# Kernel tuning notes

Hardware: AMD Instinct MI355X
Metric: run time of the kernel (lower is better)

The kernel has to match this reference:

```python
import jax, jax.numpy as jnp
import numpy as np

H = 12
DH = 64
R = 8
LN_EPS = 1e-12


def setup_inputs() -> dict:
    key = jax.random.key(0)
    ks = jax.random.split(key, 6)
    B, T, D = 32, 512, 768
    s = 0.02  # realistic init scale so softmax/LN stay well-conditioned
    return {
        "hidden_states": jax.random.normal(ks[0], (B, T, D), jnp.float32),
        "Wq": jax.random.normal(ks[1], (D, D), jnp.float32) * s,
        "bq": jnp.zeros((D,), jnp.float32),
        "Wk": jax.random.normal(ks[2], (D, D), jnp.float32) * s,
        "bk": jnp.zeros((D,), jnp.float32),
        "Wv": jax.random.normal(ks[3], (D, D), jnp.float32) * s,
        "bv": jnp.zeros((D,), jnp.float32),
        "Wo": jax.random.normal(ks[4], (D, D), jnp.float32) * s,
        "bo": jnp.zeros((D,), jnp.float32),
        "ln_g": jnp.ones((D,), jnp.float32),
        "ln_b": jnp.zeros((D,), jnp.float32),
    }


def _bipartite_indices(metric, r):
    # metric: (B, T, dh); cosine-sim bipartite matching between even (a) and odd (b) tokens
    m = metric / (jnp.linalg.norm(metric, axis=-1, keepdims=True) + 1e-6)
    a, b = m[:, ::2], m[:, 1::2]
    scores = jnp.einsum('bad,bcd->bac', a, b)  # (B, Ta, Tb)
    node_max = scores.max(axis=-1)
    node_idx = scores.argmax(axis=-1)
    node_max = node_max.at[:, 0].set(-jnp.inf)  # protect CLS (a[0])
    r = min(r, a.shape[1] - 1)
    sorted_idx = jnp.argsort(-node_max, axis=-1)  # descending
    src_idx = sorted_idx[:, :r]
    unm_idx = sorted_idx[:, r:]
    dst_idx = jnp.take_along_axis(node_idx, src_idx, axis=-1)
    return src_idx, unm_idx, dst_idx


def _merge(x, src_idx, unm_idx, dst_idx):
    # x: (B, T, C) -> (B, T - r, C); scatter-mean matched even tokens into odd tokens
    src, dst = x[:, ::2], x[:, 1::2]
    matched = jnp.take_along_axis(src, src_idx[:, :, None], axis=1)  # (B, r, C)

    def scat(d, di, mm):
        sums = jnp.zeros_like(d).at[di].add(mm)
        cnt = jnp.zeros((d.shape[0],), d.dtype).at[di].add(jnp.ones(di.shape, d.dtype))
        # torch scatter_reduce 'mean' with include_self=True: (self + sum) / (1 + count)
        return (d + sums) / (1.0 + cnt[:, None])

    dst = jax.vmap(scat)(dst, dst_idx, matched)
    unm = jnp.take_along_axis(src, unm_idx[:, :, None], axis=1)
    return jnp.concatenate([unm, dst], axis=1)


def reference(hidden_states, Wq, bq, Wk, bk, Wv, bv, Wo, bo, ln_g, ln_b):
    B, T, D = hidden_states.shape

    def split_heads(x):
        return x.reshape(B, T, H, DH).transpose(0, 2, 1, 3)  # (B, H, T, dh)

    residual = hidden_states
    q = split_heads(hidden_states @ Wq + bq)
    k = split_heads(hidden_states @ Wk + bk)
    v = split_heads(hidden_states @ Wv + bv)

    # ToMe: match on head-averaged keys (computed under no_grad in torch)
    metric = jax.lax.stop_gradient(k.mean(axis=1))  # (B, T, dh)
    src_idx, unm_idx, dst_idx = _bipartite_indices(metric, R)

    def merge_heads(x):
        Bx, Hx, Tx, dx = x.shape
        y = x.transpose(0, 2, 1, 3).reshape(Bx, Tx, Hx * dx)
        y = _merge(y, src_idx, unm_idx, dst_idx)
        return y.reshape(Bx, y.shape[1], Hx, dx).transpose(0, 2, 1, 3)

    q = merge_heads(q)
    k = merge_heads(k)
    v = merge_heads(v)
    residual = _merge(residual, src_idx, unm_idx, dst_idx)

    scores = jnp.einsum('bhqd,bhkd->bhqk', q, k) / jnp.sqrt(jnp.float32(DH))
    probs = jax.nn.softmax(scores, axis=-1)  # dropout is identity in eval
    ctx = jnp.einsum('bhqk,bhkd->bhqd', probs, v)
    T2 = ctx.shape[2]
    ctx = ctx.transpose(0, 2, 1, 3).reshape(B, T2, D)
    out = ctx @ Wo + bo

    x = out + residual
    mu = x.mean(axis=-1, keepdims=True)
    var = x.var(axis=-1, keepdims=True)
    return (x - mu) / jnp.sqrt(var + LN_EPS) * ln_g + ln_b
```

## Files before the change

kernel.cpp:

```cpp
#include <hip/hip_runtime.h>
#include <math.h>

#define BNUM 32
#define TT   512
#define DD   768
#define HH   12
#define DHH  64
#define RR   8
#define TSRC 256
#define UNM  248
#define TM   504
#define MROW 16128

typedef unsigned short u16;
typedef unsigned int   u32;
typedef __attribute__((ext_vector_type(8))) short bfrag;
typedef __attribute__((ext_vector_type(4))) float ffrag;

__device__ __forceinline__ u16 f2bf(float f) {
  u32 u = __float_as_uint(f);
  u = (u + 0x7fffu + ((u >> 16) & 1u)) >> 16;
  return (u16)u;
}
__device__ __forceinline__ u32 pack2bf(float a, float b) {
  u32 ua = __float_as_uint(a), ub = __float_as_uint(b);
  ua += 0x7fffu + ((ua >> 16) & 1u);
  ub += 0x7fffu + ((ub >> 16) & 1u);
  return (ua >> 16) | (ub & 0xffff0000u);
}
__device__ __forceinline__ float bf2f(u16 v) {
  return __uint_as_float(((u32)v) << 16);
}

__device__ __forceinline__ void gl2lds16(const u16* g, u16* l) {
  __builtin_amdgcn_global_load_lds(
      (const __attribute__((address_space(1))) void*)(g),
      (__attribute__((address_space(3))) void*)(l), 16, 0, 0);
}

__global__ __launch_bounds__(256) void wkr_kernel(
    const float* __restrict__ Wk, const float* __restrict__ bk,
    float* __restrict__ Wkr, float* __restrict__ bkr) {
  int idx = blockIdx.x * 256 + threadIdx.x;
  int d = idx >> 6, j = idx & 63;
  float s = 0.f;
  #pragma unroll
  for (int h = 0; h < HH; ++h) s += Wk[(size_t)d * DD + h * DHH + j];
  Wkr[idx] = s * (1.f / 12.f);
  if (idx < 64) {
    float sb = 0.f;
    #pragma unroll
    for (int h = 0; h < HH; ++h) sb += bk[h * DHH + idx];
    bkr[idx] = sb * (1.f / 12.f);
  }
}

__global__ __launch_bounds__(256) void gemm_f32_kernel(
    const float* __restrict__ A, const float* __restrict__ W,
    const float* __restrict__ bias, float* __restrict__ C,
    int M, int N, int K) {
  __shared__ float As[32][34];
  __shared__ float Ws[32][66];
  const int t  = threadIdx.x;
  const int m0 = blockIdx.x * 32;
  const int tx = t & 15, ty = t >> 4;
  const int a_kk = t & 31;
  const int a_m  = t >> 5;
  const int w_n  = t & 63;
  const int w_k0 = t >> 6;

  float a_pre[4], w_pre[8];
  #pragma unroll
  for (int l = 0; l < 4; ++l)
    a_pre[l] = A[(size_t)(m0 + a_m + 8 * l) * K + a_kk];
  #pragma unroll
  for (int l = 0; l < 8; ++l)
    w_pre[l] = W[(size_t)(w_k0 * 8 + l) * N + w_n];

  float4 acc0 = make_float4(0.f, 0.f, 0.f, 0.f);
  float4 acc1 = make_float4(0.f, 0.f, 0.f, 0.f);

  for (int k0 = 0; k0 < K; k0 += 32) {
    __syncthreads();
    #pragma unroll
    for (int l = 0; l < 4; ++l) As[a_kk][a_m + 8 * l] = a_pre[l];
    #pragma unroll
    for (int l = 0; l < 8; ++l) Ws[w_k0 * 8 + l][w_n] = w_pre[l];
    __syncthreads();
    if (k0 + 32 < K) {
      #pragma unroll
      for (int l = 0; l < 4; ++l)
        a_pre[l] = A[(size_t)(m0 + a_m + 8 * l) * K + k0 + 32 + a_kk];
      #pragma unroll
      for (int l = 0; l < 8; ++l)
        w_pre[l] = W[(size_t)(k0 + 32 + w_k0 * 8 + l) * N + w_n];
    }
    #pragma unroll
    for (int kk = 0; kk < 32; ++kk) {
      float2 a2 = *(const float2*)&As[kk][ty * 2];
      float4 w4 = *(const float4*)&Ws[kk][tx * 4];
      acc0.x += a2.x * w4.x; acc0.y += a2.x * w4.y; acc0.z += a2.x * w4.z; acc0.w += a2.x * w4.w;
      acc1.x += a2.y * w4.x; acc1.y += a2.y * w4.y; acc1.z += a2.y * w4.z; acc1.w += a2.y * w4.w;
    }
  }
  const float4 b4 = *(const float4*)&bias[tx * 4];
  float4 v0 = acc0, v1 = acc1;
  v0.x += b4.x; v0.y += b4.y; v0.z += b4.z; v0.w += b4.w;
  v1.x += b4.x; v1.y += b4.y; v1.z += b4.z; v1.w += b4.w;
  *(float4*)&C[(size_t)(m0 + ty * 2) * N + tx * 4]     = v0;
  *(float4*)&C[(size_t)(m0 + ty * 2 + 1) * N + tx * 4] = v1;
}

__global__ __launch_bounds__(256) void wconv_kernel(
    const float* __restrict__ W0, const float* __restrict__ W1,
    const float* __restrict__ W2, const float* __restrict__ W3,
    u16* __restrict__ T0, u16* __restrict__ T1,
    u16* __restrict__ T2, u16* __restrict__ T3) {
  __shared__ float tile[64][65];
  int wi = blockIdx.z;
  const float* W = (wi == 0) ? W0 : (wi == 1) ? W1 : (wi == 2) ? W2 : W3;
  u16* T = (wi == 0) ? T0 : (wi == 1) ? T1 : (wi == 2) ? T2 : T3;
  int k0 = blockIdx.x * 64, n0 = blockIdx.y * 64;
  int t = threadIdx.x;
  int r = t >> 2, c4 = (t & 3) * 16;
  #pragma unroll
  for (int j = 0; j < 16; j += 4) {
    float4 v = *(const float4*)&W[(size_t)(k0 + r) * DD + n0 + c4 + j];
    tile[r][c4 + j] = v.x; tile[r][c4 + j + 1] = v.y;
    tile[r][c4 + j + 2] = v.z; tile[r][c4 + j + 3] = v.w;
  }
  __syncthreads();
  #pragma unroll
  for (int j = 0; j < 16; j += 2) {
    u32 p = (u32)f2bf(tile[c4 + j][r]) | ((u32)f2bf(tile[c4 + j + 1][r]) << 16);
    *(u32*)&T[(size_t)(n0 + r) * DD + k0 + c4 + j] = p;
  }
}

template <bool OUT_BF16, bool ADD_RES, bool ROW_BIAS>
__global__ __launch_bounds__(256) void mfma_gemm_kernel(
    const u16* __restrict__ A, const u16* __restrict__ BT,
    const float* __restrict__ bias, const float* __restrict__ Res,
    float* __restrict__ Cf, u16* __restrict__ Cb,
    int M, int N, int K) {
  __shared__ u16 Als[128 * 64];
  __shared__ u16 Bls[128 * 64];
  const int t  = threadIdx.x;
  const int m0 = blockIdx.x * 128;
  const int n0 = blockIdx.y * 128;
  const int lane = t & 63;
  const int w  = t >> 6;
  const int wm = w & 1, wn = w >> 1;
  const int q  = lane >> 4;
  const int lr = lane & 15;

  const int srow = lane >> 3;
  const int schk = (lane & 7) ^ srow;
  const u16* gA = A  + (size_t)(m0 + w * 32 + srow) * K + schk * 8;
  const u16* gB = BT + (size_t)(n0 + w * 32 + srow) * K + schk * 8;
  u16* lA = &Als[(w * 32) * 64];
  u16* lB = &Bls[(w * 32) * 64];

  const int rchk0 = (q)     ^ (lr & 7);
  const int rchk1 = (4 + q) ^ (lr & 7);

  ffrag acc[4][4];
  #pragma unroll
  for (int i = 0; i < 4; ++i)
    #pragma unroll
    for (int j = 0; j < 4; ++j) {
      acc[i][j].x = 0.f; acc[i][j].y = 0.f; acc[i][j].z = 0.f; acc[i][j].w = 0.f;
    }

  for (int k0 = 0; k0 < K; k0 += 64) {
    __syncthreads();
    #pragma unroll
    for (int i = 0; i < 4; ++i) {
      gl2lds16(gA + (size_t)(i * 8) * K + k0, lA + i * 8 * 64);
      gl2lds16(gB + (size_t)(i * 8) * K + k0, lB + i * 8 * 64);
    }
    __syncthreads();

    bfrag af[2][4], bfv[2][4];
    #pragma unroll
    for (int mi = 0; mi < 4; ++mi) {
      const u16* ra = &Als[(wm * 64 + mi * 16 + lr) * 64];
      af[0][mi] = *(const bfrag*)(ra + rchk0 * 8);
      af[1][mi] = *(const bfrag*)(ra + rchk1 * 8);
    }
    #pragma unroll
    for (int ni = 0; ni < 4; ++ni) {
      const u16* rb = &Bls[(wn * 64 + ni * 16 + lr) * 64];
      bfv[0][ni] = *(const bfrag*)(rb + rchk0 * 8);
      bfv[1][ni] = *(const bfrag*)(rb + rchk1 * 8);
    }
    #pragma unroll
    for (int s = 0; s < 2; ++s)
      #pragma unroll
      for (int mi = 0; mi < 4; ++mi)
        #pragma unroll
        for (int ni = 0; ni < 4; ++ni)
          acc[mi][ni] = __builtin_amdgcn_mfma_f32_16x16x32_bf16(
              af[s][mi], bfv[s][ni], acc[mi][ni], 0, 0, 0);
  }

  float bcol[4];
  if (!ROW_BIAS) {
    #pragma unroll
    for (int ni = 0; ni < 4; ++ni)
      bcol[ni] = bias[n0 + wn * 64 + ni * 16 + lr];
  }

  #pragma unroll
  for (int mi = 0; mi < 4; ++mi) {
    #pragma unroll
    for (int ni = 0; ni < 4; ++ni) {
      int gcol = n0 + wn * 64 + ni * 16 + lr;
      #pragma unroll
      for (int r = 0; r < 4; ++r) {
        int grow = m0 + wm * 64 + mi * 16 + q * 4 + r;
        size_t off = (size_t)grow * N + gcol;
        float v = acc[mi][ni][r];
        v += ROW_BIAS ? bias[grow] : bcol[ni];
        if (ADD_RES) v += Res[off];
        if (OUT_BF16) Cb[off] = f2bf(v);
        else          Cf[off] = v;
      }
    }
  }
}

__global__ __launch_bounds__(256) void tome_kernel(
    const float* __restrict__ metric, int* __restrict__ order_g,
    int* __restrict__ dst_g) {
  __shared__ float sm[TSRC * 64];
  int b = blockIdx.x, i = threadIdx.x;
  const float* Mb = metric + (size_t)b * TT * 64;

  float areg[64];
  float na = 0.f;
  #pragma unroll
  for (int d = 0; d < 64; ++d) {
    float v = Mb[(size_t)(2 * i) * 64 + d];
    areg[d] = v; na += v * v;
  }
  float ia = 1.f / (sqrtf(na) + 1e-6f);
  #pragma unroll
  for (int d = 0; d < 64; ++d) areg[d] *= ia;

  float nb = 0.f;
  #pragma unroll
  for (int d = 0; d < 64; ++d) {
    float v = Mb[(size_t)(2 * i + 1) * 64 + d];
    sm[i * 64 + d] = v; nb += v * v;
  }
  float ib = 1.f / (sqrtf(nb) + 1e-6f);
  #pragma unroll
  for (int d = 0; d < 64; ++d) sm[i * 64 + d] *= ib;
  __syncthreads();

  float best = -INFINITY; int besti = 0;
  for (int c = 0; c < TSRC; ++c) {
    float s = 0.f;
    #pragma unroll
    for (int d = 0; d < 64; ++d) s += areg[d] * sm[c * 64 + d];
    if (s > best) { best = s; besti = c; }
  }
  if (i == 0) best = -INFINITY;
  __syncthreads();

  sm[i] = best;
  int* smi = (int*)(sm + TSRC);
  smi[i] = besti;
  __syncthreads();

  float ki = sm[i];
  int r = 0;
  for (int j = 0; j < TSRC; ++j) {
    float kj = sm[j];
    if (kj > ki || (kj == ki && j < i)) ++r;
  }
  int* ord = smi + TSRC;
  ord[r] = i;
  __syncthreads();

  order_g[b * TSRC + i] = ord[i];
  if (i < RR) dst_g[b * RR + i] = smi[ord[i]];
}

__global__ __launch_bounds__(256) void merge_kernel(
    const float* __restrict__ X, const int* __restrict__ order,
    const int* __restrict__ dsti, float* __restrict__ Xm,
    u16* __restrict__ Xmb) {
  int row = blockIdx.x;
  int b = row / TM, t2 = row % TM;
  int c = threadIdx.x;
  const float* Xb = X + (size_t)b * TT * DD;
  float out[3];
  if (t2 < UNM) {
    int tok = 2 * order[b * TSRC + RR + t2];
    #pragma unroll
    for (int l = 0; l < 3; ++l) out[l] = Xb[(size_t)tok * DD + c + 256 * l];
  } else {
    int j = t2 - UNM;
    float cnt = 1.f;
    #pragma unroll
    for (int l = 0; l < 3; ++l) out[l] = Xb[(size_t)(2 * j + 1) * DD + c + 256 * l];
    for (int m = 0; m < RR; ++m) {
      if (dsti[b * RR + m] == j) {
        int tok = 2 * order[b * TSRC + m];
        #pragma unroll
        for (int l = 0; l < 3; ++l) out[l] += Xb[(size_t)tok * DD + c + 256 * l];
        cnt += 1.f;
      }
    }
    float inv = 1.f / cnt;
    #pragma unroll
    for (int l = 0; l < 3; ++l) out[l] *= inv;
  }
  #pragma unroll
  for (int l = 0; l < 3; ++l) {
    Xm[(size_t)row * DD + c + 256 * l]  = out[l];
    Xmb[(size_t)row * DD + c + 256 * l] = f2bf(out[l]);
  }
}

#define NQT 8
__global__ __launch_bounds__(256) void attn_kernel(
    const u16* __restrict__ Q, const u16* __restrict__ K,
    const u16* __restrict__ VT, u16* __restrict__ ctx) {
  __shared__ u16 Kls[2][64][64];
  __shared__ u16 Vls[2][64][64];
  __shared__ u16 Pt[64][72];

  int blk = blockIdx.x;
  int bh = blk % (BNUM * HH);
  int qt = blk / (BNUM * HH);
  int h = bh % HH, b = bh / HH;
  const int t = threadIdx.x;
  const int lane = t & 63, w = t >> 6;
  const int lr = lane & 15, quad = lane >> 4;
  const int q0 = qt * 64;
  const size_t base = (size_t)b * TM * DD + (size_t)h * DHH;

  bfrag qf[2];
  {
    const u16* qp = Q + base + (size_t)(q0 + 16 * w + lr) * DD + quad * 8;
    qf[0] = *(const bfrag*)(qp);
    qf[1] = *(const bfrag*)(qp + 32);
  }

  const int srow = lane >> 3;
  const int schk = (lane & 7) ^ srow;
  const u16* Kg = K + base + (size_t)schk * 8;
  const u16* Vg0 = VT + (size_t)(h * DHH + w * 16 + srow) * MROW + (size_t)b * TM;
  const u16* Vg1 = Vg0 + (size_t)8 * MROW;

  const int cA = (quad)     ^ (lr & 7);
  const int cB = (quad + 4) ^ (lr & 7);

  float m_i = -INFINITY, l_i = 0.f;
  ffrag o[4];
  #pragma unroll
  for (int ni = 0; ni < 4; ++ni) {
    o[ni].x = 0.f; o[ni].y = 0.f; o[ni].z = 0.f; o[ni].w = 0.f;
  }

  auto STAGE = [&](int cur, int kt) {
    const int k0s = kt * 64;
    int t0 = k0s + w * 16 + srow;
    int t1 = t0 + 8;
    t0 = (t0 < TM) ? t0 : (TM - 1);
    t1 = (t1 < TM) ? t1 : (TM - 1);
    gl2lds16(Kg + (size_t)t0 * DD, &Kls[cur][w * 16][0]);
    gl2lds16(Kg + (size_t)t1 * DD, &Kls[cur][w * 16 + 8][0]);
    int tb = k0s + schk * 8;
    tb = (tb <= TM - 8) ? tb : (TM - 8);
    gl2lds16(Vg0 + tb, &Vls[cur][w * 16][0]);
    gl2lds16(Vg1 + tb, &Vls[cur][w * 16 + 8][0]);
  };

  STAGE(0, 0);
  __syncthreads();

  const float L2E = 1.4426950408889634f;
  const float C1  = 0.125f * 1.4426950408889634f;

  #pragma unroll
  for (int kt = 0; kt < NQT; ++kt) {
    const int cur = kt & 1;

    if (kt + 1 < NQT) STAGE(cur ^ 1, kt + 1);

    ffrag s4[4];
    __builtin_amdgcn_s_setprio(1);
    #pragma unroll
    for (int mi = 0; mi < 4; ++mi) {
      bfrag ka0 = *(const bfrag*)&Kls[cur][mi * 16 + lr][cA * 8];
      bfrag ka1 = *(const bfrag*)&Kls[cur][mi * 16 + lr][cB * 8];
      ffrag z; z.x = 0.f; z.y = 0.f; z.z = 0.f; z.w = 0.f;
      z = __builtin_amdgcn_mfma_f32_16x16x32_bf16(ka0, qf[0], z, 0, 0, 0);
      s4[mi] = __builtin_amdgcn_mfma_f32_16x16x32_bf16(ka1, qf[1], z, 0, 0, 0);
    }
    __builtin_amdgcn_s_setprio(0);

    if (kt == NQT - 1) {
      #pragma unroll
      for (int mi = 0; mi < 4; ++mi)
        #pragma unroll
        for (int r = 0; r < 4; ++r) {
          int rel = mi * 16 + quad * 4 + r;
          if (mi == 3)
            s4[mi][r] = (448 + rel < TM) ? s4[mi][r] : -INFINITY;
        }
    }

    float mx01 = fmaxf(fmaxf(s4[0][0], s4[0][1]), fmaxf(s4[0][2], s4[0][3]));
    float mx23 = fmaxf(fmaxf(s4[1][0], s4[1][1]), fmaxf(s4[1][2], s4[1][3]));
    float mx45 = fmaxf(fmaxf(s4[2][0], s4[2][1]), fmaxf(s4[2][2], s4[2][3]));
    float mx67 = fmaxf(fmaxf(s4[3][0], s4[3][1]), fmaxf(s4[3][2], s4[3][3]));
    float rmax = fmaxf(fmaxf(mx01, mx23), fmaxf(mx45, mx67));
    rmax = fmaxf(rmax, __shfl_xor(rmax, 16));
    rmax = fmaxf(rmax, __shfl_xor(rmax, 32));
    float nm = fmaxf(m_i, rmax * 0.125f);
    float alpha = __builtin_amdgcn_exp2f((m_i - nm) * L2E);
    float nml2 = nm * L2E;

    float p[16];
    float pa0 = 0.f, pa1 = 0.f, pa2 = 0.f, pa3 = 0.f;
    #pragma unroll
    for (int mi = 0; mi < 4; ++mi)
      #pragma unroll
      for (int r = 0; r < 4; ++r) {
        float e = __builtin_amdgcn_exp2f(__builtin_fmaf(s4[mi][r], C1, -nml2));
        p[mi * 4 + r] = e;
        if (r == 0) pa0 += e; else if (r == 1) pa1 += e;
        else if (r == 2) pa2 += e; else pa3 += e;
      }
    float psum = (pa0 + pa1) + (pa2 + pa3);
    psum += __shfl_xor(psum, 16);
    psum += __shfl_xor(psum, 32);
    l_i = l_i * alpha + psum;
    m_i = nm;

    #pragma unroll
    for (int mi = 0; mi < 4; ++mi) {
      u32 lo = pack2bf(p[mi * 4 + 0], p[mi * 4 + 1]);
      u32 hi = pack2bf(p[mi * 4 + 2], p[mi * 4 + 3]);
      u32* dst = (u32*)&Pt[16 * w + lr][mi * 16 + quad * 4];
      dst[0] = lo; dst[1] = hi;
    }

    float al[4];
    #pragma unroll
    for (int r = 0; r < 4; ++r) al[r] = __shfl(alpha, quad * 4 + r);
    #pragma unroll
    for (int ni = 0; ni < 4; ++ni)
      #pragma unroll
      for (int r = 0; r < 4; ++r) o[ni][r] *= al[r];

    bfrag pfa0 = *(const bfrag*)&Pt[16 * w + lr][quad * 8];
    bfrag pfa1 = *(const bfrag*)&Pt[16 * w + lr][32 + quad * 8];
    __builtin_amdgcn_s_setprio(1);
    #pragma unroll
    for (int ni = 0; ni < 4; ++ni) {
      bfrag vb0 = *(const bfrag*)&Vls[cur][ni * 16 + lr][cA * 8];
      bfrag vb1 = *(const bfrag*)&Vls[cur][ni * 16 + lr][cB * 8];
      o[ni] = __builtin_amdgcn_mfma_f32_16x16x32_bf16(pfa0, vb0, o[ni], 0, 0, 0);
      o[ni] = __builtin_amdgcn_mfma_f32_16x16x32_bf16(pfa1, vb1, o[ni], 0, 0, 0);
    }
    __builtin_amdgcn_s_setprio(0);

    __syncthreads();
  }

  float invl[4];
  #pragma unroll
  for (int r = 0; r < 4; ++r) {
    float lv = __shfl(l_i, quad * 4 + r);
    invl[r] = 1.f / lv;
  }
  #pragma unroll
  for (int r = 0; r < 4; ++r) {
    int row = q0 + 16 * w + quad * 4 + r;
    if (row < TM) {
      size_t g = base + (size_t)row * DD + lr;
      #pragma unroll
      for (int ni = 0; ni < 4; ++ni)
        ctx[g + ni * 16] = f2bf(o[ni][r] * invl[r]);
    }
  }
}

__global__ __launch_bounds__(256) void ln_kernel(
    float* __restrict__ Y, const float* __restrict__ g,
    const float* __restrict__ beta) {
  __shared__ float red[4];
  int row = blockIdx.x, t = threadIdx.x;
  size_t baseo = (size_t)row * DD;
  float x[3];
  #pragma unroll
  for (int l = 0; l < 3; ++l) x[l] = Y[baseo + t + 256 * l];
  float s = x[0] + x[1] + x[2];
  #pragma unroll
  for (int off = 32; off > 0; off >>= 1) s += __shfl_down(s, off, 64);
  if ((t & 63) == 0) red[t >> 6] = s;
  __syncthreads();
  float mu = (red[0] + red[1] + red[2] + red[3]) * (1.f / 768.f);
  __syncthreads();
  float d0 = x[0] - mu, d1 = x[1] - mu, d2 = x[2] - mu;
  float sq = d0 * d0 + d1 * d1 + d2 * d2;
  #pragma unroll
  for (int off = 32; off > 0; off >>= 1) sq += __shfl_down(sq, off, 64);
  if ((t & 63) == 0) red[t >> 6] = sq;
  __syncthreads();
  float var = (red[0] + red[1] + red[2] + red[3]) * (1.f / 768.f);
  float inv = rsqrtf(var + 1e-12f);
  #pragma unroll
  for (int l = 0; l < 3; ++l) {
    int c = t + 256 * l;
    Y[baseo + c] = (x[l] - mu) * inv * g[c] + beta[c];
  }
}

extern "C" void kernel_launch(void* const* d_in, const int* in_sizes, int n_in,
                              void* d_out, int out_size, void* d_ws, size_t ws_size,
                              hipStream_t stream) {
  const float* X    = (const float*)d_in[0];
  const float* Wq   = (const float*)d_in[1];
  const float* bq   = (const float*)d_in[2];
  const float* Wk   = (const float*)d_in[3];
  const float* bk   = (const float*)d_in[4];
  const float* Wv   = (const float*)d_in[5];
  const float* bv   = (const float*)d_in[6];
  const float* Wo   = (const float*)d_in[7];
  const float* bo   = (const float*)d_in[8];
  const float* ln_g = (const float*)d_in[9];
  const float* ln_b = (const float*)d_in[10];
  float* out = (float*)d_out;

  const size_t metric_n = (size_t)16384 * 64;
  const size_t wkr_n    = (size_t)768 * 64 + 64;
  const size_t idx_n    = (size_t)BNUM * TSRC + BNUM * RR;
  const size_t buf_n    = (size_t)MROW * DD;
  const size_t w_n      = (size_t)DD * DD;
  const size_t f32_elems = metric_n + wkr_n + idx_n + buf_n;
  const size_t u16_elems = 4 * buf_n + 4 * w_n;
  const size_t needed = f32_elems * 4 + u16_elems * 2;
  if (ws_size < needed) return;

  float* ws = (float*)d_ws;
  float* metric  = ws;
  float* Wkr     = metric + metric_n;
  float* bkr     = Wkr + (size_t)768 * 64;
  int*   order_g = (int*)(bkr + 64);
  int*   dst_g   = order_g + BNUM * TSRC;
  float* Xm      = (float*)(dst_g + BNUM * RR);
  u16*   Xmb     = (u16*)(Xm + buf_n);
  u16*   Qmb     = Xmb + buf_n;
  u16*   Kmb     = Qmb + buf_n;
  u16*   VTb     = Kmb + buf_n;
  u16*   WqT     = VTb + buf_n;
  u16*   WkT     = WqT + w_n;
  u16*   WvT     = WkT + w_n;
  u16*   WoT     = WvT + w_n;
  u16*   ctxb    = Qmb;

  wkr_kernel<<<(768 * 64) / 256, 256, 0, stream>>>(Wk, bk, Wkr, bkr);
  wconv_kernel<<<dim3(12, 12, 4), 256, 0, stream>>>(
      Wq, Wk, Wv, Wo, WqT, WkT, WvT, WoT);
  gemm_f32_kernel<<<dim3(16384 / 32, 1), 256, 0, stream>>>(
      X, Wkr, bkr, metric, 16384, 64, 768);
  tome_kernel<<<BNUM, 256, 0, stream>>>(metric, order_g, dst_g);
  merge_kernel<<<MROW, 256, 0, stream>>>(X, order_g, dst_g, Xm, Xmb);
  mfma_gemm_kernel<true, false, false><<<dim3(MROW / 128, DD / 128), 256, 0, stream>>>(
      Xmb, WqT, bq, nullptr, nullptr, Qmb, MROW, DD, DD);
  mfma_gemm_kernel<true, false, false><<<dim3(MROW / 128, DD / 128), 256, 0, stream>>>(
      Xmb, WkT, bk, nullptr, nullptr, Kmb, MROW, DD, DD);
  mfma_gemm_kernel<true, false, true><<<dim3(DD / 128, MROW / 128), 256, 0, stream>>>(
      WvT, Xmb, bv, nullptr, nullptr, VTb, DD, MROW, DD);
  attn_kernel<<<BNUM * HH * NQT, 256, 0, stream>>>(Qmb, Kmb, VTb, ctxb);
  mfma_gemm_kernel<false, true, false><<<dim3(MROW / 128, DD / 128), 256, 0, stream>>>(
      ctxb, WoT, bo, Xm, out, nullptr, MROW, DD, DD);
  ln_kernel<<<MROW, 256, 0, stream>>>(out, ln_g, ln_b);
}
```

Before: 453.2 us.

## Double-buffer GEMM LDS tiles and fuse Q/K projections into one launch

The MFMA GEMM now loads K-slices of 32 into two alternating LDS buffers. The next slice is staged while the current one is multiplied, so each iteration needs one barrier instead of two. The Q and K projections run as a single launch with twice as many column blocks, which relies on WkT sitting directly after WqT in memory. Launch bounds now request 4 blocks per CU. The trade is more frequent K-loop iterations with smaller MFMA batches and a new swizzle scheme, plus possible register pressure from the occupancy hint.

```diff
diff --git a/kernel.cpp b/kernel.cpp
--- a/kernel.cpp
+++ b/kernel.cpp
@@ -137,14 +137,15 @@
   }
 }
 
-template <bool OUT_BF16, bool ADD_RES, bool ROW_BIAS>
-__global__ __launch_bounds__(256) void mfma_gemm_kernel(
+template <bool OUT_BF16, bool ADD_RES, bool ROW_BIAS, bool QK>
+__global__ __launch_bounds__(256, 4) void mfma_gemm_kernel(
     const u16* __restrict__ A, const u16* __restrict__ BT,
-    const float* __restrict__ bias, const float* __restrict__ Res,
-    float* __restrict__ Cf, u16* __restrict__ Cb,
+    const float* __restrict__ bias, const float* __restrict__ bias2,
+    const float* __restrict__ Res,
+    float* __restrict__ Cf, u16* __restrict__ Cb, u16* __restrict__ Cb2,
     int M, int N, int K) {
-  __shared__ u16 Als[128 * 64];
-  __shared__ u16 Bls[128 * 64];
+  __shared__ u16 Als[2][128 * 32];
+  __shared__ u16 Bls[2][128 * 32];
   const int t  = threadIdx.x;
   const int m0 = blockIdx.x * 128;
   const int n0 = blockIdx.y * 128;
@@ -154,15 +155,17 @@
   const int q  = lane >> 4;
   const int lr = lane & 15;
 
-  const int srow = lane >> 3;
-  const int schk = (lane & 7) ^ srow;
+  const int srow = lane >> 2;
+  const int schk = (lane & 3) ^ ((lane >> 3) & 3);
   const u16* gA = A  + (size_t)(m0 + w * 32 + srow) * K + schk * 8;
   const u16* gB = BT + (size_t)(n0 + w * 32 + srow) * K + schk * 8;
-  u16* lA = &Als[(w * 32) * 64];
-  u16* lB = &Bls[(w * 32) * 64];
-
-  const int rchk0 = (q)     ^ (lr & 7);
-  const int rchk1 = (4 + q) ^ (lr & 7);
+
+  const int ceff = q ^ ((lr >> 1) & 3);
+
+  const float* biasp = bias;
+  u16* Cbp = Cb;
+  int n0c = n0;
+  if (QK && n0 >= DD) { biasp = bias2; Cbp = Cb2; n0c = n0 - DD; }
 
   ffrag acc[4][4];
   #pragma unroll
@@ -172,50 +175,51 @@
       acc[i][j].x = 0.f; acc[i][j].y = 0.f; acc[i][j].z = 0.f; acc[i][j].w = 0.f;
     }
 
-  for (int k0 = 0; k0 < K; k0 += 64) {
+  auto STAGE = [&](int buf, int k0) {
+    #pragma unroll
+    for (int i = 0; i < 2; ++i) {
+      gl2lds16(gA + (size_t)(i * 16) * K + k0, &Als[buf][(w * 32 + i * 16) * 32]);
+      gl2lds16(gB + (size_t)(i * 16) * K + k0, &Bls[buf][(w * 32 + i * 16) * 32]);
+    }
+  };
+
+  STAGE(0, 0);
+  __syncthreads();
+
+  const int NK = K >> 5;
+  for (int kt = 0; kt < NK; ++kt) {
+    const int cur = kt & 1;
+    if (kt + 1 < NK) STAGE(cur ^ 1, (kt + 1) << 5);
+
+    bfrag af[4], bfv[4];
+    #pragma unroll
+    for (int mi = 0; mi < 4; ++mi)
+      af[mi] = *(const bfrag*)&Als[cur][((wm * 4 + mi) * 64 + lr * 4 + ceff) * 8];
+    #pragma unroll
+    for (int ni = 0; ni < 4; ++ni)
+      bfv[ni] = *(const bfrag*)&Bls[cur][((wn * 4 + ni) * 64 + lr * 4 + ceff) * 8];
+    #pragma unroll
+    for (int mi = 0; mi < 4; ++mi)
+      #pragma unroll
+      for (int ni = 0; ni < 4; ++ni)
+        acc[mi][ni] = __builtin_amdgcn_mfma_f32_16x16x32_bf16(
+            af[mi], bfv[ni], acc[mi][ni], 0, 0, 0);
+
     __syncthreads();
-    #pragma unroll
-    for (int i = 0; i < 4; ++i) {
-      gl2lds16(gA + (size_t)(i * 8) * K + k0, lA + i * 8 * 64);
-      gl2lds16(gB + (size_t)(i * 8) * K + k0, lB + i * 8 * 64);
-    }
-    __syncthreads();
-
-    bfrag af[2][4], bfv[2][4];
-    #pragma unroll
-    for (int mi = 0; mi < 4; ++mi) {
-      const u16* ra = &Als[(wm * 64 + mi * 16 + lr) * 64];
-      af[0][mi] = *(const bfrag*)(ra + rchk0 * 8);
-      af[1][mi] = *(const bfrag*)(ra + rchk1 * 8);
-    }
-    #pragma unroll
-    for (int ni = 0; ni < 4; ++ni) {
-      const u16* rb = &Bls[(wn * 64 + ni * 16 + lr) * 64];
-      bfv[0][ni] = *(const bfrag*)(rb + rchk0 * 8);
-      bfv[1][ni] = *(const bfrag*)(rb + rchk1 * 8);
-    }
-    #pragma unroll
-    for (int s = 0; s < 2; ++s)
-      #pragma unroll
-      for (int mi = 0; mi < 4; ++mi)
-        #pragma unroll
-        for (int ni = 0; ni < 4; ++ni)
-          acc[mi][ni] = __builtin_amdgcn_mfma_f32_16x16x32_bf16(
-              af[s][mi], bfv[s][ni], acc[mi][ni], 0, 0, 0);
   }
 
   float bcol[4];
   if (!ROW_BIAS) {
     #pragma unroll
     for (int ni = 0; ni < 4; ++ni)
-      bcol[ni] = bias[n0 + wn * 64 + ni * 16 + lr];
+      bcol[ni] = biasp[n0c + wn * 64 + ni * 16 + lr];
   }
 
   #pragma unroll
   for (int mi = 0; mi < 4; ++mi) {
     #pragma unroll
     for (int ni = 0; ni < 4; ++ni) {
-      int gcol = n0 + wn * 64 + ni * 16 + lr;
+      int gcol = n0c + wn * 64 + ni * 16 + lr;
       #pragma unroll
       for (int r = 0; r < 4; ++r) {
         int grow = m0 + wm * 64 + mi * 16 + q * 4 + r;
@@ -223,7 +227,7 @@
         float v = acc[mi][ni][r];
         v += ROW_BIAS ? bias[grow] : bcol[ni];
         if (ADD_RES) v += Res[off];
-        if (OUT_BF16) Cb[off] = f2bf(v);
+        if (OUT_BF16) Cbp[off] = f2bf(v);
         else          Cf[off] = v;
       }
     }
@@ -573,14 +577,15 @@
       X, Wkr, bkr, metric, 16384, 64, 768);
   tome_kernel<<<BNUM, 256, 0, stream>>>(metric, order_g, dst_g);
   merge_kernel<<<MROW, 256, 0, stream>>>(X, order_g, dst_g, Xm, Xmb);
-  mfma_gemm_kernel<true, false, false><<<dim3(MROW / 128, DD / 128), 256, 0, stream>>>(
-      Xmb, WqT, bq, nullptr, nullptr, Qmb, MROW, DD, DD);
-  mfma_gemm_kernel<true, false, false><<<dim3(MROW / 128, DD / 128), 256, 0, stream>>>(
-      Xmb, WkT, bk, nullptr, nullptr, Kmb, MROW, DD, DD);
-  mfma_gemm_kernel<true, false, true><<<dim3(DD / 128, MROW / 128), 256, 0, stream>>>(
-      WvT, Xmb, bv, nullptr, nullptr, VTb, DD, MROW, DD);
+  mfma_gemm_kernel<true, false, false, true>
+      <<<dim3(MROW / 128, 2 * DD / 128), 256, 0, stream>>>(
+      Xmb, WqT, bq, bk, nullptr, nullptr, Qmb, Kmb, MROW, DD, DD);
+  mfma_gemm_kernel<true, false, true, false>
+      <<<dim3(DD / 128, MROW / 128), 256, 0, stream>>>(
+      WvT, Xmb, bv, nullptr, nullptr, nullptr, VTb, nullptr, DD, MROW, DD);
   attn_kernel<<<BNUM * HH * NQT, 256, 0, stream>>>(Qmb, Kmb, VTb, ctxb);
-  mfma_gemm_kernel<false, true, false><<<dim3(MROW / 128, DD / 128), 256, 0, stream>>>(
-      ctxb, WoT, bo, Xm, out, nullptr, MROW, DD, DD);
+  mfma_gemm_kernel<false, true, false, false>
+      <<<dim3(MROW / 128, DD / 128), 256, 0, stream>>>(
+      ctxb, WoT, bo, nullptr, Xm, out, nullptr, nullptr, MROW, DD, DD);
   ln_kernel<<<MROW, 256, 0, stream>>>(out, ln_g, ln_b);
 }
```

Result: no change. 458.9 us (+1.2%).
